# Kernel tuning notes

Measured on AMD Instinct MI355X. Metric: run time of the kernel, lower is better.

Reference implementation:

```python
import jax, jax.numpy as jnp
import numpy as np

TAU = 2.0
THRESHOLD = 1.0
STEPS = 20


def lif_layer(x_seq, W, b):
    """x_seq: [B, T, F_in]; W: [F_out, F_in]; b: [F_out].
    Returns (final membrane [B, F_out], spike train [B, T, F_out])."""
    # One batched GEMM for all timesteps (same math as per-step nn.Linear).
    inp = jnp.einsum('btf,of->bto', x_seq, W) + b  # [B, T, O]
    B, T, O = inp.shape

    def step(mem, inp_t):
        mem = mem + (inp_t - mem) / TAU
        spk = (mem >= THRESHOLD).astype(mem.dtype)
        mem = mem * (1.0 - spk)
        return mem, spk

    mem_final, spks = jax.lax.scan(step, jnp.zeros((B, O), inp.dtype),
                                   jnp.swapaxes(inp, 0, 1))
    return mem_final, jnp.swapaxes(spks, 0, 1)  # [B,O], [B,T,O]


def poisson_encode(x, key):
    # torch.bernoulli(x.unsqueeze(1).expand(-1, steps, -1))
    B, F = x.shape
    p = jnp.broadcast_to(x[:, None, :], (B, STEPS, F))
    return jax.random.bernoulli(key, p).astype(x.dtype)  # [B, T, F]


def setup_inputs() -> dict:
    key = jax.random.key(0)
    ks = jax.random.split(key, 8)
    B, F_IN, H1, H2, OUT = 4096, 2000, 512, 128, 10
    s = 0.02
    return {
        'x': jax.random.uniform(ks[0], (B, F_IN), dtype=jnp.float32),
        'W1': jax.random.normal(ks[1], (H1, F_IN), dtype=jnp.float32) * s,
        'b1': jnp.zeros((H1,), jnp.float32),
        'W2': jax.random.normal(ks[2], (H2, H1), dtype=jnp.float32) * s,
        'b2': jnp.zeros((H2,), jnp.float32),
        'Wd': jax.random.normal(ks[3], (OUT, H2), dtype=jnp.float32) * s,
        'bd': jnp.zeros((OUT,), jnp.float32),
    }


def reference(x, W1, b1, W2, b2, Wd, bd):
    spike_train = poisson_encode(x, jax.random.key(1))  # [B, T, 2000]
    mem1, spk1 = lif_layer(spike_train, W1, b1)          # spk1: [B, T, 512]
    mem2, spk2 = lif_layer(spk1, W2, b2)                 # mem2: [B, 128]
    return mem2 @ Wd.T + bd                              # [B, 10]
```

## Files before the change

### kernel.cpp

```cpp
#include <hip/hip_runtime.h>
#include <stdint.h>

typedef int i32x4  __attribute__((ext_vector_type(4)));
typedef int i32x16 __attribute__((ext_vector_type(16)));

constexpr int Bsz  = 4096;
constexpr int Tst  = 20;
constexpr int Fin  = 2000;
constexpr int H1   = 512;
constexpr int H2   = 128;
constexpr int NOUT = 10;
constexpr int FW   = 64;

#define TFR(r) { x0 += x1; x1 = __builtin_rotateleft32(x1, (r)) ^ x0; }
__device__ __forceinline__ uint32_t tf_bits(uint32_t c1) {
  const uint32_t k1 = 1u, k2 = 0x1BD11BDBu;
  uint32_t x0 = 0u, x1 = c1 + k1;
  TFR(13) TFR(15) TFR(26) TFR(6)   x0 += k1; x1 += k2 + 1u;
  TFR(17) TFR(29) TFR(16) TFR(24)  x0 += k2; x1 += 2u;
  TFR(13) TFR(15) TFR(26) TFR(6)              x1 += k1 + 3u;
  TFR(17) TFR(29) TFR(16) TFR(24)  x0 += k1; x1 += k2 + 4u;
  TFR(13) TFR(15) TFR(26) TFR(6)   x0 += k2; x1 += 5u;
  return x0 ^ x1;
}
#undef TFR

__global__ __launch_bounds__(256) void spikegen4(const float* __restrict__ x,
                                                 uint32_t* __restrict__ sbits) {
  int gid = blockIdx.x * 256 + threadIdx.x;
  int w8 = gid & 255;
  int b  = gid >> 8;
  int f0 = w8 * 8;
  const float* xr = x + (size_t)b * Fin;
  uint32_t T[8];
#pragma unroll
  for (int j = 0; j < 8; ++j) {
    int f = f0 + j;
    float p = (f < Fin) ? xr[f] : 0.0f;
    T[j] = (uint32_t)ceilf(p * 8388608.0f);
    asm volatile("" : "+v"(T[j]));
  }
  uint8_t* sb = (uint8_t*)sbits + (size_t)(b * Tst) * 256 + w8;
  uint32_t ib = (uint32_t)(b * Tst) * (uint32_t)Fin + (uint32_t)f0;
#pragma unroll 1
  for (int t = 0; t < Tst; ++t) {
    uint32_t bits = 0;
#pragma unroll
    for (int j = 0; j < 8; ++j) {
      uint32_t m = tf_bits(ib + (uint32_t)j) >> 9;
      bits |= ((m - T[j]) >> 31) << j;
    }
    *sb = (uint8_t)bits;
    sb += 256;
    ib += (uint32_t)Fin;
  }
}

__global__ void wslice_i8(const float* __restrict__ W, int O, int K, int KPAD,
                          int8_t* __restrict__ Btl) {
  int idx = blockIdx.x * 256 + threadIdx.x;
  if (idx >= O * KPAD) return;
  int o = idx / KPAD, f = idx % KPAD;
  long long wi = 0;
  if (f < K) wi = llround((double)W[(size_t)o * K + f] * 8589934592.0);
  int nt = o >> 5, c = o & 31, kst = f >> 5, kh = (f >> 4) & 1, j = f & 15;
  int NT = O >> 5, KST = KPAD >> 5;
  size_t base = (((size_t)nt * KST + kst) << 10) + (size_t)(kh * 32 + c) * 16 + j;
  size_t sstride = ((size_t)NT * KST) << 10;
  long long rem = wi;
#pragma unroll
  for (int s = 0; s < 4; ++s) {
    int d;
    if (s < 3) { d = (int)(int8_t)(rem & 0xff); rem = (rem - d) >> 8; }
    else d = (int)rem;
    Btl[base + (size_t)s * sstride] = (int8_t)d;
  }
}

typedef const __attribute__((address_space(1))) uint32_t* gas_ptr;
typedef __attribute__((address_space(3))) uint32_t* las_ptr;
__device__ __forceinline__ void gld16(const void* g, void* l) {
  __builtin_amdgcn_global_load_lds((gas_ptr)g, (las_ptr)l, 16, 0, 0);
}

__device__ __forceinline__ i32x4 expand16(uint32_t m) {
  const uint32_t MUL = 0x00204081u, MSK = 0x01010101u;
  uint4 v = make_uint4(
      ((m         & 0xFu) * MUL) & MSK,
      (((m >> 4)  & 0xFu) * MUL) & MSK,
      (((m >> 8)  & 0xFu) * MUL) & MSK,
      (((m >> 12) & 0xFu) * MUL) & MSK);
  return __builtin_bit_cast(i32x4, v);
}

template <int KPAD, int O>
__global__ __launch_bounds__(256, 4) void gemm_i8(
    const uint32_t* __restrict__ Abits, int awords, int rowBase,
    const int8_t* __restrict__ Btl, const float* __restrict__ bias,
    float* __restrict__ Cout) {
  constexpr int KST = KPAD / 32;
  constexpr int NR  = KST / 2;
  constexpr int NT  = O / 32;
  __shared__ __align__(16) char smem[32768];
  const int tid = threadIdx.x;
  const int lane = tid & 63;
  const int s = tid >> 6;
  const int row0 = blockIdx.x * 64;
  const int col0 = blockIdx.y * 64;
  const int nt0 = blockIdx.y * 2;
  const int lrow = lane & 31;
  const int shA = (lane >> 5) * 16;

  i32x16 acc[2][2] = {};

  const int rstride = awords * 4;
  const uint8_t* ar0 = (const uint8_t*)Abits + (size_t)(rowBase + row0 + lrow) * rstride;
  const uint8_t* ar1 = ar0 + (size_t)32 * rstride;
  const int8_t* bsrc0 = Btl + ((((size_t)s * NT + nt0) * KST) << 10) + (size_t)lane * 16;
  const int8_t* bsrc1 = Btl + ((((size_t)s * NT + nt0 + 1) * KST) << 10) + (size_t)lane * 16;
  char* sBs = smem + s * 8192;

#define STAGE(buf, r) do {                                                                 \
    gld16(bsrc0 + ((size_t)(2*(r))   << 10), sBs + (buf) * 4096 +        lane * 16);       \
    gld16(bsrc1 + ((size_t)(2*(r))   << 10), sBs + (buf) * 4096 + 1024 + lane * 16);       \
    gld16(bsrc0 + ((size_t)(2*(r)+1) << 10), sBs + (buf) * 4096 + 2048 + lane * 16);       \
    gld16(bsrc1 + ((size_t)(2*(r)+1) << 10), sBs + (buf) * 4096 + 3072 + lane * 16);       \
  } while (0)

#define ROUND(r, WAITN, w0m0, w1m0, w0m1, w1m1, DO_STAGE, DO_A4N, gnext) do {              \
    asm volatile("s_waitcnt vmcnt(" #WAITN ")" ::: "memory");                              \
    __builtin_amdgcn_sched_barrier(0);                                                     \
    const char* bb = sBs + ((r) & 1) * 4096 + lane * 16;                                   \
    uint4 b00 = *(const uint4*)(bb);                                                       \
    uint4 b01 = *(const uint4*)(bb + 1024);                                                \
    uint4 b10 = *(const uint4*)(bb + 2048);                                                \
    uint4 b11 = *(const uint4*)(bb + 3072);                                                \
    asm volatile("s_waitcnt lgkmcnt(0)" ::: "memory");                                     \
    if (DO_STAGE) STAGE((r) & 1, (r) + 2);                                                 \
    if (DO_A4N) {                                                                          \
      A40n = *(const uint4*)(ar0 + (size_t)(gnext) * 16);                                  \
      A41n = *(const uint4*)(ar1 + (size_t)(gnext) * 16);                                  \
    }                                                                                      \
    i32x4 a00 = expand16(w0m0 >> shA);                                        \
    i32x4 a01 = expand16(w1m0 >> shA);                                        \
    i32x4 a10 = expand16(w0m1 >> shA);                                        \
    i32x4 a11 = expand16(w1m1 >> shA);                                        \
    i32x4 c00 = __builtin_bit_cast(i32x4, b00), c01 = __builtin_bit_cast(i32x4, b01);      \
    i32x4 c10 = __builtin_bit_cast(i32x4, b10), c11 = __builtin_bit_cast(i32x4, b11);      \
    __builtin_amdgcn_s_setprio(1);                                                         \
    acc[0][0] = __builtin_amdgcn_mfma_i32_32x32x32_i8(a00, c00, acc[0][0], 0, 0, 0);       \
    acc[0][1] = __builtin_amdgcn_mfma_i32_32x32x32_i8(a00, c01, acc[0][1], 0, 0, 0);       \
    acc[1][0] = __builtin_amdgcn_mfma_i32_32x32x32_i8(a10, c00, acc[1][0], 0, 0, 0);       \
    acc[1][1] = __builtin_amdgcn_mfma_i32_32x32x32_i8(a10, c01, acc[1][1], 0, 0, 0);       \
    acc[0][0] = __builtin_amdgcn_mfma_i32_32x32x32_i8(a01, c10, acc[0][0], 0, 0, 0);       \
    acc[0][1] = __builtin_amdgcn_mfma_i32_32x32x32_i8(a01, c11, acc[0][1], 0, 0, 0);       \
    acc[1][0] = __builtin_amdgcn_mfma_i32_32x32x32_i8(a11, c10, acc[1][0], 0, 0, 0);       \
    acc[1][1] = __builtin_amdgcn_mfma_i32_32x32x32_i8(a11, c11, acc[1][1], 0, 0, 0);       \
    __builtin_amdgcn_s_setprio(0);                                                         \
  } while (0)

  STAGE(0, 0);
  STAGE(1, 1);
  uint4 A40 = *(const uint4*)(ar0);
  uint4 A41 = *(const uint4*)(ar1);
  uint4 A40n, A41n;

#pragma unroll 1
  for (int g = 0; g < NR / 2 - 1; ++g) {
    ROUND(2 * g,     4, A40.x, A40.y, A41.x, A41.y, true, true, g + 1);
    ROUND(2 * g + 1, 4, A40.z, A40.w, A41.z, A41.w, true, false, 0);
    A40 = A40n; A41 = A41n;
  }
  ROUND(NR - 2, 4, A40.x, A40.y, A41.x, A41.y, false, false, 0);
  ROUND(NR - 1, 0, A40.z, A40.w, A41.z, A41.w, false, false, 0);
#undef ROUND
#undef STAGE

  int* red = (int*)smem;
#pragma unroll
  for (int n = 0; n < 2; ++n) {
    __syncthreads();
#pragma unroll
    for (int m = 0; m < 2; ++m)
#pragma unroll
      for (int r = 0; r < 16; ++r) {
        int row = m * 32 + (r & 3) + ((r >> 2) << 3) + ((lane >> 5) << 2);
        red[(s * 64 + row) * 32 + (lane & 31)] = acc[m][n][r];
      }
    __syncthreads();
    for (int e = tid; e < 2048; e += 256) {
      int row = e >> 5, c = e & 31;
      long long v = 0;
#pragma unroll
      for (int s4 = 0; s4 < 4; ++s4)
        v += (long long)red[(s4 * 64 + row) * 32 + c] * (1LL << (8 * s4));
      int col = col0 + n * 32 + c;
      Cout[(size_t)(row0 + row) * O + col] = (float)((double)v * 0x1p-33 + (double)bias[col]);
    }
  }
}

__global__ __launch_bounds__(512) void lif1(const float* __restrict__ inp1,
                                            uint32_t* __restrict__ spk1, int bBase) {
  int b_local = blockIdx.x;
  int o = threadIdx.x;
  int b = bBase + b_local;
  double mem = 0.0;
  for (int t = 0; t < Tst; ++t) {
    double inp = (double)inp1[((size_t)(b_local * Tst + t)) * H1 + o];
    mem = mem + (inp - mem) / 2.0;
    bool spk = (mem >= 1.0);
    unsigned long long m = __ballot(spk);
    if ((o & 63) == 0) {
      int wv = o >> 6;
      size_t base = ((size_t)(b * Tst + t)) * (H1 / 32);
      spk1[base + wv * 2]     = (uint32_t)(m & 0xffffffffu);
      spk1[base + wv * 2 + 1] = (uint32_t)(m >> 32);
    }
    if (spk) mem = 0.0;
  }
}

__global__ __launch_bounds__(128) void lif2(const float* __restrict__ inp2,
                                            double* __restrict__ mem2, int bBase) {
  int b_local = blockIdx.x;
  int o = threadIdx.x;
  double mem = 0.0;
  for (int t = 0; t < Tst; ++t) {
    double inp = (double)inp2[((size_t)(b_local * Tst + t)) * H2 + o];
    mem = mem + (inp - mem) / 2.0;
    if (mem >= 1.0) mem = 0.0;
  }
  mem2[(size_t)(bBase + b_local) * H2 + o] = mem;
}

__global__ void finalk(const double* __restrict__ mem2, const float* __restrict__ Wd,
                       const float* __restrict__ bd, float* __restrict__ out) {
  int gid = blockIdx.x * blockDim.x + threadIdx.x;
  if (gid >= Bsz * NOUT) return;
  int b = gid / NOUT, j = gid % NOUT;
  double s = (double)bd[j];
  const double* m = mem2 + (size_t)b * H2;
  const float* wr = Wd + (size_t)j * H2;
  for (int k = 0; k < H2; ++k) s = fma(m[k], (double)wr[k], s);
  out[gid] = (float)s;
}

extern "C" void kernel_launch(void* const* d_in, const int* in_sizes, int n_in,
                              void* d_out, int out_size, void* d_ws, size_t ws_size,
                              hipStream_t stream) {
  const float* x  = (const float*)d_in[0];
  const float* W1 = (const float*)d_in[1];
  const float* b1 = (const float*)d_in[2];
  const float* W2 = (const float*)d_in[3];
  const float* b2 = (const float*)d_in[4];
  const float* Wd = (const float*)d_in[5];
  const float* bd = (const float*)d_in[6];
  float* out = (float*)d_out;

  char* ws = (char*)d_ws;
  float*    inp   = (float*)   (ws);
  double*   mem2  = (double*)  (ws + 41943040ull);
  uint32_t* sbits = (uint32_t*)(ws + 46137344ull);
  uint32_t* spk1  = (uint32_t*)(ws + 67108864ull);
  int8_t*   Btl1  = (int8_t*)  (ws + 72351744ull);
  int8_t*   Btl2  = (int8_t*)  (ws + 77594624ull);

  spikegen4<<<dim3(Bsz), dim3(256), 0, stream>>>(x, sbits);

  wslice_i8<<<dim3(512 * 2048 / 256), dim3(256), 0, stream>>>(W1, 512, 2000, 2048, Btl1);
  wslice_i8<<<dim3(128 * 512 / 256),  dim3(256), 0, stream>>>(W2, 128, 512, 512, Btl2);

  for (int c = 0; c < 4; ++c) {
    gemm_i8<2048, 512><<<dim3(320, 8), dim3(256), 0, stream>>>(
        sbits, FW, c * 20480, Btl1, b1, inp);
    lif1<<<dim3(1024), dim3(H1), 0, stream>>>(inp, spk1, c * 1024);
  }

  for (int c = 0; c < 2; ++c) {
    gemm_i8<512, 128><<<dim3(640, 2), dim3(256), 0, stream>>>(
        spk1, H1 / 32, c * 40960, Btl2, b2, inp);
    lif2<<<dim3(2048), dim3(H2), 0, stream>>>(inp, mem2, c * 2048);
  }

  finalk<<<dim3((Bsz * NOUT + 255) / 256), dim3(256), 0, stream>>>(mem2, Wd, bd, out);
}
```

Baseline: 852.1 us.

## Pre-expand spike bits to int8 tiles and load GEMM operands directly to registers

Adds a separate kernel that expands packed spike bits into MFMA-ready int8 tiles in workspace. The GEMM then loads both A and B straight from global memory into registers with a two-stage double buffer, dropping LDS staging for B and the in-loop bit expansion. Each block now computes a 64x128 tile with four column MFMA groups, and the batch is split into smaller chunks. The cost is an extra kernel pass per chunk, plus the expanded A written to and re-read from memory at 8x the size of the packed bits. The GEMM also runs at lower occupancy and holds more registers.

```diff
diff --git a/kernel.cpp b/kernel.cpp
--- a/kernel.cpp
+++ b/kernel.cpp
@@ -77,108 +77,93 @@
   }
 }
 
-typedef const __attribute__((address_space(1))) uint32_t* gas_ptr;
-typedef __attribute__((address_space(3))) uint32_t* las_ptr;
-__device__ __forceinline__ void gld16(const void* g, void* l) {
-  __builtin_amdgcn_global_load_lds((gas_ptr)g, (las_ptr)l, 16, 0, 0);
-}
-
-__device__ __forceinline__ i32x4 expand16(uint32_t m) {
+__device__ __forceinline__ uint4 expand16u(uint32_t m) {
   const uint32_t MUL = 0x00204081u, MSK = 0x01010101u;
-  uint4 v = make_uint4(
+  return make_uint4(
       ((m         & 0xFu) * MUL) & MSK,
       (((m >> 4)  & 0xFu) * MUL) & MSK,
       (((m >> 8)  & 0xFu) * MUL) & MSK,
       (((m >> 12) & 0xFu) * MUL) & MSK);
-  return __builtin_bit_cast(i32x4, v);
+}
+
+template <int KST>
+__global__ __launch_bounds__(256) void aexp(const uint32_t* __restrict__ bits,
+                                            int awords, int rowBase,
+                                            uint8_t* __restrict__ Ai8) {
+  int tid = blockIdx.x * 256 + threadIdx.x;
+  int L = tid & 63;
+  int idx = tid >> 6;
+  int m = idx & 1;
+  int rk = idx >> 1;
+  int kst = rk & (KST - 1);
+  int rt = rk / KST;
+  int row = rowBase + rt * 64 + m * 32 + (L & 31);
+  uint32_t b16 = *(const uint16_t*)((const uint8_t*)bits +
+                  (size_t)row * (size_t)(awords * 4) + kst * 4 + (L >> 5) * 2);
+  *(uint4*)(Ai8 + (size_t)tid * 16) = expand16u(b16);
 }
 
 template <int KPAD, int O>
-__global__ __launch_bounds__(256, 4) void gemm_i8(
-    const uint32_t* __restrict__ Abits, int awords, int rowBase,
-    const int8_t* __restrict__ Btl, const float* __restrict__ bias,
-    float* __restrict__ Cout) {
+__global__ __launch_bounds__(256, 2) void gemm_i8v2(
+    const uint8_t* __restrict__ Ai8, const int8_t* __restrict__ Btl,
+    const float* __restrict__ bias, float* __restrict__ Cout) {
   constexpr int KST = KPAD / 32;
   constexpr int NR  = KST / 2;
   constexpr int NT  = O / 32;
-  __shared__ __align__(16) char smem[32768];
+  __shared__ __align__(16) int red[4 * 64 * 32];
   const int tid = threadIdx.x;
   const int lane = tid & 63;
   const int s = tid >> 6;
-  const int row0 = blockIdx.x * 64;
-  const int col0 = blockIdx.y * 64;
-  const int nt0 = blockIdx.y * 2;
-  const int lrow = lane & 31;
-  const int shA = (lane >> 5) * 16;
-
-  i32x16 acc[2][2] = {};
-
-  const int rstride = awords * 4;
-  const uint8_t* ar0 = (const uint8_t*)Abits + (size_t)(rowBase + row0 + lrow) * rstride;
-  const uint8_t* ar1 = ar0 + (size_t)32 * rstride;
-  const int8_t* bsrc0 = Btl + ((((size_t)s * NT + nt0) * KST) << 10) + (size_t)lane * 16;
-  const int8_t* bsrc1 = Btl + ((((size_t)s * NT + nt0 + 1) * KST) << 10) + (size_t)lane * 16;
-  char* sBs = smem + s * 8192;
-
-#define STAGE(buf, r) do {                                                                 \
-    gld16(bsrc0 + ((size_t)(2*(r))   << 10), sBs + (buf) * 4096 +        lane * 16);       \
-    gld16(bsrc1 + ((size_t)(2*(r))   << 10), sBs + (buf) * 4096 + 1024 + lane * 16);       \
-    gld16(bsrc0 + ((size_t)(2*(r)+1) << 10), sBs + (buf) * 4096 + 2048 + lane * 16);       \
-    gld16(bsrc1 + ((size_t)(2*(r)+1) << 10), sBs + (buf) * 4096 + 3072 + lane * 16);       \
+  const int rt = blockIdx.x;
+  const int nt0 = blockIdx.y * 4;
+
+  const uint8_t* asrc = Ai8 + ((size_t)rt * KST * 2) * 1024 + (size_t)lane * 16;
+  const int8_t*  bsrc = Btl + (((size_t)s * NT + nt0) * KST) * 1024 + (size_t)lane * 16;
+
+  i32x16 acc[2][4] = {};
+  uint4 A0[2][2], B0[2][4], A1[2][2], B1[2][4];
+
+#define LOADG(Ar, Br, r) do {                                                        \
+    _Pragma("unroll") for (int kk = 0; kk < 2; ++kk) {                               \
+      _Pragma("unroll") for (int mm = 0; mm < 2; ++mm)                               \
+        Ar[kk][mm] = *(const uint4*)(asrc + (((size_t)(2*(r)+kk) * 2 + mm) << 10));  \
+      _Pragma("unroll") for (int nn = 0; nn < 4; ++nn)                               \
+        Br[kk][nn] = *(const uint4*)(bsrc + (((size_t)nn * KST + 2*(r)+kk) << 10));  \
+    }                                                                                \
   } while (0)
 
-#define ROUND(r, WAITN, w0m0, w1m0, w0m1, w1m1, DO_STAGE, DO_A4N, gnext) do {              \
-    asm volatile("s_waitcnt vmcnt(" #WAITN ")" ::: "memory");                              \
-    __builtin_amdgcn_sched_barrier(0);                                                     \
-    const char* bb = sBs + ((r) & 1) * 4096 + lane * 16;                                   \
-    uint4 b00 = *(const uint4*)(bb);                                                       \
-    uint4 b01 = *(const uint4*)(bb + 1024);                                                \
-    uint4 b10 = *(const uint4*)(bb + 2048);                                                \
-    uint4 b11 = *(const uint4*)(bb + 3072);                                                \
-    asm volatile("s_waitcnt lgkmcnt(0)" ::: "memory");                                     \
-    if (DO_STAGE) STAGE((r) & 1, (r) + 2);                                                 \
-    if (DO_A4N) {                                                                          \
-      A40n = *(const uint4*)(ar0 + (size_t)(gnext) * 16);                                  \
-      A41n = *(const uint4*)(ar1 + (size_t)(gnext) * 16);                                  \
-    }                                                                                      \
-    i32x4 a00 = expand16(w0m0 >> shA);                                        \
-    i32x4 a01 = expand16(w1m0 >> shA);                                        \
-    i32x4 a10 = expand16(w0m1 >> shA);                                        \
-    i32x4 a11 = expand16(w1m1 >> shA);                                        \
-    i32x4 c00 = __builtin_bit_cast(i32x4, b00), c01 = __builtin_bit_cast(i32x4, b01);      \
-    i32x4 c10 = __builtin_bit_cast(i32x4, b10), c11 = __builtin_bit_cast(i32x4, b11);      \
-    __builtin_amdgcn_s_setprio(1);                                                         \
-    acc[0][0] = __builtin_amdgcn_mfma_i32_32x32x32_i8(a00, c00, acc[0][0], 0, 0, 0);       \
-    acc[0][1] = __builtin_amdgcn_mfma_i32_32x32x32_i8(a00, c01, acc[0][1], 0, 0, 0);       \
-    acc[1][0] = __builtin_amdgcn_mfma_i32_32x32x32_i8(a10, c00, acc[1][0], 0, 0, 0);       \
-    acc[1][1] = __builtin_amdgcn_mfma_i32_32x32x32_i8(a10, c01, acc[1][1], 0, 0, 0);       \
-    acc[0][0] = __builtin_amdgcn_mfma_i32_32x32x32_i8(a01, c10, acc[0][0], 0, 0, 0);       \
-    acc[0][1] = __builtin_amdgcn_mfma_i32_32x32x32_i8(a01, c11, acc[0][1], 0, 0, 0);       \
-    acc[1][0] = __builtin_amdgcn_mfma_i32_32x32x32_i8(a11, c10, acc[1][0], 0, 0, 0);       \
-    acc[1][1] = __builtin_amdgcn_mfma_i32_32x32x32_i8(a11, c11, acc[1][1], 0, 0, 0);       \
-    __builtin_amdgcn_s_setprio(0);                                                         \
+#define ROUND(Ar, Br, WAITN) do {                                                   \
+    asm volatile("s_waitcnt vmcnt(" #WAITN ")" ::: "memory");                        \
+    __builtin_amdgcn_s_setprio(1);                                                   \
+    _Pragma("unroll") for (int kk = 0; kk < 2; ++kk) {                               \
+      i32x4 a0 = __builtin_bit_cast(i32x4, Ar[kk][0]);                               \
+      i32x4 a1 = __builtin_bit_cast(i32x4, Ar[kk][1]);                               \
+      _Pragma("unroll") for (int nn = 0; nn < 4; ++nn) {                             \
+        i32x4 bv = __builtin_bit_cast(i32x4, Br[kk][nn]);                            \
+        acc[0][nn] = __builtin_amdgcn_mfma_i32_32x32x32_i8(a0, bv, acc[0][nn], 0, 0, 0); \
+        acc[1][nn] = __builtin_amdgcn_mfma_i32_32x32x32_i8(a1, bv, acc[1][nn], 0, 0, 0); \
+      }                                                                              \
+    }                                                                                \
+    __builtin_amdgcn_s_setprio(0);                                                   \
   } while (0)
 
-  STAGE(0, 0);
-  STAGE(1, 1);
-  uint4 A40 = *(const uint4*)(ar0);
-  uint4 A41 = *(const uint4*)(ar1);
-  uint4 A40n, A41n;
+  LOADG(A0, B0, 0);
+  LOADG(A1, B1, 1);
 
 #pragma unroll 1
   for (int g = 0; g < NR / 2 - 1; ++g) {
-    ROUND(2 * g,     4, A40.x, A40.y, A41.x, A41.y, true, true, g + 1);
-    ROUND(2 * g + 1, 4, A40.z, A40.w, A41.z, A41.w, true, false, 0);
-    A40 = A40n; A41 = A41n;
-  }
-  ROUND(NR - 2, 4, A40.x, A40.y, A41.x, A41.y, false, false, 0);
-  ROUND(NR - 1, 0, A40.z, A40.w, A41.z, A41.w, false, false, 0);
+    ROUND(A0, B0, 12);
+    LOADG(A0, B0, 2 * g + 2);
+    ROUND(A1, B1, 12);
+    LOADG(A1, B1, 2 * g + 3);
+  }
+  ROUND(A0, B0, 12);
+  ROUND(A1, B1, 0);
 #undef ROUND
-#undef STAGE
-
-  int* red = (int*)smem;
-#pragma unroll
-  for (int n = 0; n < 2; ++n) {
+#undef LOADG
+
+#pragma unroll
+  for (int n = 0; n < 4; ++n) {
     __syncthreads();
 #pragma unroll
     for (int m = 0; m < 2; ++m)
@@ -194,8 +179,8 @@
 #pragma unroll
       for (int s4 = 0; s4 < 4; ++s4)
         v += (long long)red[(s4 * 64 + row) * 32 + c] * (1LL << (8 * s4));
-      int col = col0 + n * 32 + c;
-      Cout[(size_t)(row0 + row) * O + col] = (float)((double)v * 0x1p-33 + (double)bias[col]);
+      int col = (nt0 + n) * 32 + c;
+      Cout[(size_t)(rt * 64 + row) * O + col] = (float)((double)v * 0x1p-33 + (double)bias[col]);
     }
   }
 }
@@ -260,27 +245,30 @@
 
   char* ws = (char*)d_ws;
   float*    inp   = (float*)   (ws);
+  uint8_t*  Ai8   = (uint8_t*) (ws + 20971520ull);
   double*   mem2  = (double*)  (ws + 41943040ull);
   uint32_t* sbits = (uint32_t*)(ws + 46137344ull);
   uint32_t* spk1  = (uint32_t*)(ws + 67108864ull);
   int8_t*   Btl1  = (int8_t*)  (ws + 72351744ull);
-  int8_t*   Btl2  = (int8_t*)  (ws + 77594624ull);
+  int8_t*   Btl2  = (int8_t*)  (ws + 76546048ull);
 
   spikegen4<<<dim3(Bsz), dim3(256), 0, stream>>>(x, sbits);
 
   wslice_i8<<<dim3(512 * 2048 / 256), dim3(256), 0, stream>>>(W1, 512, 2000, 2048, Btl1);
   wslice_i8<<<dim3(128 * 512 / 256),  dim3(256), 0, stream>>>(W2, 128, 512, 512, Btl2);
 
+  for (int c = 0; c < 8; ++c) {
+    aexp<64><<<dim3(10240 * 64 * 2 / 256), dim3(256), 0, stream>>>(
+        sbits, FW, c * 10240, Ai8);
+    gemm_i8v2<2048, 512><<<dim3(160, 4), dim3(256), 0, stream>>>(Ai8, Btl1, b1, inp);
+    lif1<<<dim3(512), dim3(H1), 0, stream>>>(inp, spk1, c * 512);
+  }
+
   for (int c = 0; c < 4; ++c) {
-    gemm_i8<2048, 512><<<dim3(320, 8), dim3(256), 0, stream>>>(
-        sbits, FW, c * 20480, Btl1, b1, inp);
-    lif1<<<dim3(1024), dim3(H1), 0, stream>>>(inp, spk1, c * 1024);
-  }
-
-  for (int c = 0; c < 2; ++c) {
-    gemm_i8<512, 128><<<dim3(640, 2), dim3(256), 0, stream>>>(
-        spk1, H1 / 32, c * 40960, Btl2, b2, inp);
-    lif2<<<dim3(2048), dim3(H2), 0, stream>>>(inp, mem2, c * 2048);
+    aexp<16><<<dim3(20480 * 16 * 2 / 256), dim3(256), 0, stream>>>(
+        spk1, H1 / 32, c * 20480, Ai8);
+    gemm_i8v2<512, 128><<<dim3(320, 1), dim3(256), 0, stream>>>(Ai8, Btl2, b2, inp);
+    lif2<<<dim3(1024), dim3(H2), 0, stream>>>(inp, mem2, c * 1024);
   }
 
   finalk<<<dim3((Bsz * NOUT + 255) / 256), dim3(256), 0, stream>>>(mem2, Wd, bd, out);
```

Result: slower. 1.055 ms (+23.8%).

## Pre-expand spike bits to int8 MFMA layout in a separate pass before GEMM

Applied to the files above, without the earlier changes.

Adds an aexp kernel that expands the packed spike bitmasks into int8 tiles already laid out in MFMA operand order. The GEMM then loads A operands directly as 16-byte vectors and no longer does the multiply/mask bit expansion in its inner loop. Chunk sizes are halved (8 and 4 chunks) so the expanded buffer fits in the workspace, and Btl2 is moved. In exchange the A operand becomes 8x larger in memory and there are extra kernel launches and more global traffic.

```diff
diff --git a/kernel.cpp b/kernel.cpp
--- a/kernel.cpp
+++ b/kernel.cpp
@@ -77,27 +77,42 @@
   }
 }
 
+__device__ __forceinline__ uint4 expand16u(uint32_t m) {
+  const uint32_t MUL = 0x00204081u, MSK = 0x01010101u;
+  return make_uint4(
+      ((m         & 0xFu) * MUL) & MSK,
+      (((m >> 4)  & 0xFu) * MUL) & MSK,
+      (((m >> 8)  & 0xFu) * MUL) & MSK,
+      (((m >> 12) & 0xFu) * MUL) & MSK);
+}
+
+template <int KST>
+__global__ __launch_bounds__(256) void aexp(const uint32_t* __restrict__ bits,
+                                            int awords, int rowBase,
+                                            uint8_t* __restrict__ Ai8) {
+  int tid = blockIdx.x * 256 + threadIdx.x;
+  int L = tid & 63;
+  int idx = tid >> 6;
+  int m = idx & 1;
+  int rk = idx >> 1;
+  int kst = rk & (KST - 1);
+  int rt = rk / KST;
+  int row = rowBase + rt * 64 + m * 32 + (L & 31);
+  uint32_t b16 = *(const uint16_t*)((const uint8_t*)bits +
+                  (size_t)row * (size_t)(awords * 4) + kst * 4 + (L >> 5) * 2);
+  *(uint4*)(Ai8 + (size_t)tid * 16) = expand16u(b16);
+}
+
 typedef const __attribute__((address_space(1))) uint32_t* gas_ptr;
 typedef __attribute__((address_space(3))) uint32_t* las_ptr;
 __device__ __forceinline__ void gld16(const void* g, void* l) {
   __builtin_amdgcn_global_load_lds((gas_ptr)g, (las_ptr)l, 16, 0, 0);
 }
 
-__device__ __forceinline__ i32x4 expand16(uint32_t m) {
-  const uint32_t MUL = 0x00204081u, MSK = 0x01010101u;
-  uint4 v = make_uint4(
-      ((m         & 0xFu) * MUL) & MSK,
-      (((m >> 4)  & 0xFu) * MUL) & MSK,
-      (((m >> 8)  & 0xFu) * MUL) & MSK,
-      (((m >> 12) & 0xFu) * MUL) & MSK);
-  return __builtin_bit_cast(i32x4, v);
-}
-
 template <int KPAD, int O>
-__global__ __launch_bounds__(256, 4) void gemm_i8(
-    const uint32_t* __restrict__ Abits, int awords, int rowBase,
-    const int8_t* __restrict__ Btl, const float* __restrict__ bias,
-    float* __restrict__ Cout) {
+__global__ __launch_bounds__(256, 4) void gemm_i8v3(
+    const uint8_t* __restrict__ Ai8, const int8_t* __restrict__ Btl,
+    const float* __restrict__ bias, float* __restrict__ Cout) {
   constexpr int KST = KPAD / 32;
   constexpr int NR  = KST / 2;
   constexpr int NT  = O / 32;
@@ -105,29 +120,34 @@
   const int tid = threadIdx.x;
   const int lane = tid & 63;
   const int s = tid >> 6;
-  const int row0 = blockIdx.x * 64;
+  const int rt = blockIdx.x;
   const int col0 = blockIdx.y * 64;
   const int nt0 = blockIdx.y * 2;
-  const int lrow = lane & 31;
-  const int shA = (lane >> 5) * 16;
 
   i32x16 acc[2][2] = {};
 
-  const int rstride = awords * 4;
-  const uint8_t* ar0 = (const uint8_t*)Abits + (size_t)(rowBase + row0 + lrow) * rstride;
-  const uint8_t* ar1 = ar0 + (size_t)32 * rstride;
+  const uint8_t* asrc = Ai8 + ((size_t)rt * KST * 2) * 1024 + (size_t)lane * 16;
   const int8_t* bsrc0 = Btl + ((((size_t)s * NT + nt0) * KST) << 10) + (size_t)lane * 16;
   const int8_t* bsrc1 = Btl + ((((size_t)s * NT + nt0 + 1) * KST) << 10) + (size_t)lane * 16;
   char* sBs = smem + s * 8192;
 
-#define STAGE(buf, r) do {                                                                 \
+  uint4 A0[4], A1[4];
+
+#define LOADA(Ar, r) do {                                                                  \
+    Ar[0] = *(const uint4*)(asrc + (((size_t)(2*(r))     * 2 + 0) << 10));                 \
+    Ar[1] = *(const uint4*)(asrc + (((size_t)(2*(r))     * 2 + 1) << 10));                 \
+    Ar[2] = *(const uint4*)(asrc + (((size_t)(2*(r) + 1) * 2 + 0) << 10));                 \
+    Ar[3] = *(const uint4*)(asrc + (((size_t)(2*(r) + 1) * 2 + 1) << 10));                 \
+  } while (0)
+
+#define STAGEB(buf, r) do {                                                                \
     gld16(bsrc0 + ((size_t)(2*(r))   << 10), sBs + (buf) * 4096 +        lane * 16);       \
     gld16(bsrc1 + ((size_t)(2*(r))   << 10), sBs + (buf) * 4096 + 1024 + lane * 16);       \
     gld16(bsrc0 + ((size_t)(2*(r)+1) << 10), sBs + (buf) * 4096 + 2048 + lane * 16);       \
     gld16(bsrc1 + ((size_t)(2*(r)+1) << 10), sBs + (buf) * 4096 + 3072 + lane * 16);       \
   } while (0)
 
-#define ROUND(r, WAITN, w0m0, w1m0, w0m1, w1m1, DO_STAGE, DO_A4N, gnext) do {              \
+#define ROUND(r, WAITN, Acur, Anxt) do {                                                   \
     asm volatile("s_waitcnt vmcnt(" #WAITN ")" ::: "memory");                              \
     __builtin_amdgcn_sched_barrier(0);                                                     \
     const char* bb = sBs + ((r) & 1) * 4096 + lane * 16;                                   \
@@ -136,15 +156,12 @@
     uint4 b10 = *(const uint4*)(bb + 2048);                                                \
     uint4 b11 = *(const uint4*)(bb + 3072);                                                \
     asm volatile("s_waitcnt lgkmcnt(0)" ::: "memory");                                     \
-    if (DO_STAGE) STAGE((r) & 1, (r) + 2);                                                 \
-    if (DO_A4N) {                                                                          \
-      A40n = *(const uint4*)(ar0 + (size_t)(gnext) * 16);                                  \
-      A41n = *(const uint4*)(ar1 + (size_t)(gnext) * 16);                                  \
-    }                                                                                      \
-    i32x4 a00 = expand16(w0m0 >> shA);                                        \
-    i32x4 a01 = expand16(w1m0 >> shA);                                        \
-    i32x4 a10 = expand16(w0m1 >> shA);                                        \
-    i32x4 a11 = expand16(w1m1 >> shA);                                        \
+    if ((r) + 1 < NR) LOADA(Anxt, (r) + 1);                                                \
+    if ((r) + 2 < NR) STAGEB((r) & 1, (r) + 2);                                            \
+    i32x4 a00 = __builtin_bit_cast(i32x4, Acur[0]);                           \
+    i32x4 a10 = __builtin_bit_cast(i32x4, Acur[1]);                           \
+    i32x4 a01 = __builtin_bit_cast(i32x4, Acur[2]);                           \
+    i32x4 a11 = __builtin_bit_cast(i32x4, Acur[3]);                           \
     i32x4 c00 = __builtin_bit_cast(i32x4, b00), c01 = __builtin_bit_cast(i32x4, b01);      \
     i32x4 c10 = __builtin_bit_cast(i32x4, b10), c11 = __builtin_bit_cast(i32x4, b11);      \
     __builtin_amdgcn_s_setprio(1);                                                         \
@@ -159,22 +176,20 @@
     __builtin_amdgcn_s_setprio(0);                                                         \
   } while (0)
 
-  STAGE(0, 0);
-  STAGE(1, 1);
-  uint4 A40 = *(const uint4*)(ar0);
-  uint4 A41 = *(const uint4*)(ar1);
-  uint4 A40n, A41n;
+  LOADA(A0, 0);
+  STAGEB(0, 0);
+  STAGEB(1, 1);
 
 #pragma unroll 1
   for (int g = 0; g < NR / 2 - 1; ++g) {
-    ROUND(2 * g,     4, A40.x, A40.y, A41.x, A41.y, true, true, g + 1);
-    ROUND(2 * g + 1, 4, A40.z, A40.w, A41.z, A41.w, true, false, 0);
-    A40 = A40n; A41 = A41n;
-  }
-  ROUND(NR - 2, 4, A40.x, A40.y, A41.x, A41.y, false, false, 0);
-  ROUND(NR - 1, 0, A40.z, A40.w, A41.z, A41.w, false, false, 0);
+    ROUND(2 * g,     4, A0, A1);
+    ROUND(2 * g + 1, 4, A1, A0);
+  }
+  ROUND(NR - 2, 4, A0, A1);
+  ROUND(NR - 1, 0, A1, A0);
 #undef ROUND
-#undef STAGE
+#undef STAGEB
+#undef LOADA
 
   int* red = (int*)smem;
 #pragma unroll
@@ -195,7 +210,7 @@
       for (int s4 = 0; s4 < 4; ++s4)
         v += (long long)red[(s4 * 64 + row) * 32 + c] * (1LL << (8 * s4));
       int col = col0 + n * 32 + c;
-      Cout[(size_t)(row0 + row) * O + col] = (float)((double)v * 0x1p-33 + (double)bias[col]);
+      Cout[(size_t)(rt * 64 + row) * O + col] = (float)((double)v * 0x1p-33 + (double)bias[col]);
     }
   }
 }
@@ -260,27 +275,30 @@
 
   char* ws = (char*)d_ws;
   float*    inp   = (float*)   (ws);
+  uint8_t*  Ai8   = (uint8_t*) (ws + 20971520ull);
   double*   mem2  = (double*)  (ws + 41943040ull);
   uint32_t* sbits = (uint32_t*)(ws + 46137344ull);
   uint32_t* spk1  = (uint32_t*)(ws + 67108864ull);
   int8_t*   Btl1  = (int8_t*)  (ws + 72351744ull);
-  int8_t*   Btl2  = (int8_t*)  (ws + 77594624ull);
+  int8_t*   Btl2  = (int8_t*)  (ws + 76546048ull);
 
   spikegen4<<<dim3(Bsz), dim3(256), 0, stream>>>(x, sbits);
 
   wslice_i8<<<dim3(512 * 2048 / 256), dim3(256), 0, stream>>>(W1, 512, 2000, 2048, Btl1);
   wslice_i8<<<dim3(128 * 512 / 256),  dim3(256), 0, stream>>>(W2, 128, 512, 512, Btl2);
 
+  for (int c = 0; c < 8; ++c) {
+    aexp<64><<<dim3(10240 * 64 * 2 / 256), dim3(256), 0, stream>>>(
+        sbits, FW, c * 10240, Ai8);
+    gemm_i8v3<2048, 512><<<dim3(160, 8), dim3(256), 0, stream>>>(Ai8, Btl1, b1, inp);
+    lif1<<<dim3(512), dim3(H1), 0, stream>>>(inp, spk1, c * 512);
+  }
+
   for (int c = 0; c < 4; ++c) {
-    gemm_i8<2048, 512><<<dim3(320, 8), dim3(256), 0, stream>>>(
-        sbits, FW, c * 20480, Btl1, b1, inp);
-    lif1<<<dim3(1024), dim3(H1), 0, stream>>>(inp, spk1, c * 1024);
-  }
-
-  for (int c = 0; c < 2; ++c) {
-    gemm_i8<512, 128><<<dim3(640, 2), dim3(256), 0, stream>>>(
-        spk1, H1 / 32, c * 40960, Btl2, b2, inp);
-    lif2<<<dim3(2048), dim3(H2), 0, stream>>>(inp, mem2, c * 2048);
+    aexp<16><<<dim3(20480 * 16 * 2 / 256), dim3(256), 0, stream>>>(
+        spk1, H1 / 32, c * 20480, Ai8);
+    gemm_i8v3<512, 128><<<dim3(320, 2), dim3(256), 0, stream>>>(Ai8, Btl2, b2, inp);
+    lif2<<<dim3(1024), dim3(H2), 0, stream>>>(inp, mem2, c * 1024);
   }
 
   finalk<<<dim3((Bsz * NOUT + 255) / 256), dim3(256), 0, stream>>>(mem2, Wd, bd, out);
```

New measurement: 1.037 ms. 21.6% more time.
